# Kernel optimization log

Hardware: AMD Instinct MI355X
Metric: run time of the kernel (lower is better)

Reference implementation:

```python
import jax, jax.numpy as jnp
import numpy as np


def setup_inputs() -> dict:
    key = jax.random.key(0)
    ks = jax.random.split(key, 7)
    d, nq, nk = 64, 1024, 2048
    return {
        "query": jax.random.normal(ks[0], (1, d, nq), dtype=jnp.float32),
        "key": jax.random.normal(ks[1], (1, d, nk), dtype=jnp.float32),
        "value": jax.random.normal(ks[2], (1, d, nk), dtype=jnp.float32),
        # Conv1d(2d->d, k=1) weight squeezed to [d, 2d]; Conv1d(d->1, k=1) -> [1, d]
        "W1": jax.random.normal(ks[3], (d, 2 * d), dtype=jnp.float32) * (1.0 / np.sqrt(2 * d)),
        "b1": jax.random.normal(ks[4], (d,), dtype=jnp.float32) * 0.01,
        "W2": jax.random.normal(ks[5], (1, d), dtype=jnp.float32) * (1.0 / np.sqrt(d)),
        "b2": jax.random.normal(ks[6], (1,), dtype=jnp.float32) * 0.01,
    }


def reference(query, key, value, W1, b1, W2, b2):
    d = query.shape[1]
    # Split first conv weight into the query-half and key-half of the concat.
    # Conv1d with kernel 1 on cat([q_bcast, k_bcast]) == W1q @ q + W1k @ k (per pair).
    W1q, W1k = W1[:, :d], W1[:, d:]            # [h, d] each (h == d)
    qp = jnp.einsum('hd,bdq->bqh', W1q, query)  # [1, nq, h]
    kp = jnp.einsum('hd,bdk->bkh', W1k, key)    # [1, nk, h]
    # Pairwise hidden activations [1, nq, nk, h]
    h = jax.nn.relu(qp[:, :, None, :] + kp[:, None, :, :] + b1)
    scores = jnp.einsum('oh,bqkh->bqk', W2, h) + b2[0]  # [1, nq, nk]
    prob = jax.nn.softmax(scores, axis=-1)
    out = jnp.einsum('bnm,bdm->bdn', prob, value)        # [1, d, nq]
    return (out, scores)
```

## Files before the change

### kernel.cpp

```cpp
#include <hip/hip_runtime.h>


__global__ __launch_bounds__(256) void k1_proj(
    const float* __restrict__ q, const float* __restrict__ k,
    const float* __restrict__ W1, const float* __restrict__ b1,
    float* __restrict__ qp, float* __restrict__ kp)
{
  __shared__ float tile[256];
  const int t = threadIdx.x;
  const int b = blockIdx.x;
  if (b < 256) {
    const int nb = (b & 15) << 6;
    const int hb = (b >> 4) << 2;
    const int n = nb + (t & 63);
    const int h = hb + (t >> 6);
    const float* wr = W1 + h * 128;
    float acc = b1[h];
#pragma unroll
    for (int d = 0; d < 64; ++d) acc = fmaf(wr[d], q[(d << 10) + n], acc);
    tile[((t & 63) << 2) + (t >> 6)] = acc;
    __syncthreads();
    qp[((nb + (t >> 2)) << 6) + hb + (t & 3)] = tile[t];
  } else {
    const int b2 = b - 256;
    const int mb = (b2 & 31) << 6;
    const int hb = (b2 >> 5) << 2;
    const int m = mb + (t & 63);
    const int h = hb + (t >> 6);
    const float* wr = W1 + h * 128 + 64;
    float acc = 0.f;
#pragma unroll
    for (int d = 0; d < 64; ++d) acc = fmaf(wr[d], k[(d << 11) + m], acc);
    tile[((t & 63) << 2) + (t >> 6)] = acc;
    __syncthreads();
    kp[((mb + (t >> 2)) << 6) + hb + (t & 3)] = tile[t];
  }
}

__global__ __launch_bounds__(256, 2) void k2_scores(
    const float* __restrict__ qp, const float* __restrict__ kp,
    const float* __restrict__ W2, const float* __restrict__ b2p,
    float* __restrict__ scores, float* __restrict__ lpart)
{
  __shared__ float4 qS[1024];
  __shared__ float4 kS[1024];
  __shared__ float4 wS[16];
  const int t = threadIdx.x;
  const int qt = blockIdx.x >> 5;
  const int kt = blockIdx.x & 31;
  const int q0b = qt << 6, k0b = kt << 6;
  const float4* qp4 = (const float4*)qp;
  const float4* kp4 = (const float4*)kp;

#pragma unroll
  for (int i = 0; i < 4; ++i) {
    const int idx = (i << 8) + t;
    const int row = idx >> 4, c = idx & 15;
    const int cs = c ^ ((row >> 2) & 15);
    qS[(row << 4) + cs] = qp4[((q0b + row) << 4) + c];
    kS[(row << 4) + cs] = kp4[((k0b + row) << 4) + c];
  }
  if (t < 16) wS[t] = ((const float4*)W2)[t];
  __syncthreads();

  const int lane = t & 63, wave = t >> 6;
  const int lq = lane >> 4, lk = lane & 15;
  const int ql0 = (wave << 4) + (lq << 2);
  const int kl0 = lk << 2;
  const int sq = (wave << 2) | lq;

  float4 acc0 = {0,0,0,0}, acc1 = {0,0,0,0};
  float4 acc2 = {0,0,0,0}, acc3 = {0,0,0,0};

#pragma unroll 4
  for (int h4 = 0; h4 < 16; ++h4) {
    const float4 wv = wS[h4];
    const int qc = h4 ^ sq, kc = h4 ^ lk;
    const float4 q0f = qS[((ql0 + 0) << 4) + qc];
    const float4 q1f = qS[((ql0 + 1) << 4) + qc];
    const float4 q2f = qS[((ql0 + 2) << 4) + qc];
    const float4 q3f = qS[((ql0 + 3) << 4) + qc];
    const float4 k0f = kS[((kl0 + 0) << 4) + kc];
    const float4 k1f = kS[((kl0 + 1) << 4) + kc];
    const float4 k2f = kS[((kl0 + 2) << 4) + kc];
    const float4 k3f = kS[((kl0 + 3) << 4) + kc];
#define HC(C)                                                        \
    acc0.x = fmaf(wv.C, fmaxf(q0f.C + k0f.C, 0.f), acc0.x);          \
    acc0.y = fmaf(wv.C, fmaxf(q0f.C + k1f.C, 0.f), acc0.y);          \
    acc0.z = fmaf(wv.C, fmaxf(q0f.C + k2f.C, 0.f), acc0.z);          \
    acc0.w = fmaf(wv.C, fmaxf(q0f.C + k3f.C, 0.f), acc0.w);          \
    acc1.x = fmaf(wv.C, fmaxf(q1f.C + k0f.C, 0.f), acc1.x);          \
    acc1.y = fmaf(wv.C, fmaxf(q1f.C + k1f.C, 0.f), acc1.y);          \
    acc1.z = fmaf(wv.C, fmaxf(q1f.C + k2f.C, 0.f), acc1.z);          \
    acc1.w = fmaf(wv.C, fmaxf(q1f.C + k3f.C, 0.f), acc1.w);          \
    acc2.x = fmaf(wv.C, fmaxf(q2f.C + k0f.C, 0.f), acc2.x);          \
    acc2.y = fmaf(wv.C, fmaxf(q2f.C + k1f.C, 0.f), acc2.y);          \
    acc2.z = fmaf(wv.C, fmaxf(q2f.C + k2f.C, 0.f), acc2.z);          \
    acc2.w = fmaf(wv.C, fmaxf(q2f.C + k3f.C, 0.f), acc2.w);          \
    acc3.x = fmaf(wv.C, fmaxf(q3f.C + k0f.C, 0.f), acc3.x);          \
    acc3.y = fmaf(wv.C, fmaxf(q3f.C + k1f.C, 0.f), acc3.y);          \
    acc3.z = fmaf(wv.C, fmaxf(q3f.C + k2f.C, 0.f), acc3.z);          \
    acc3.w = fmaf(wv.C, fmaxf(q3f.C + k3f.C, 0.f), acc3.w);
    HC(x) HC(y) HC(z) HC(w)
#undef HC
  }

  const float b2v = b2p[0];
  float4* sc4 = (float4*)scores;
  const int kcol = (k0b >> 2) + lk;
#define ROW_OUT(I, ACC) {                                            \
    float4 s = ACC;                                                  \
    s.x += b2v; s.y += b2v; s.z += b2v; s.w += b2v;                  \
    sc4[((q0b + ql0 + I) << 9) + kcol] = s;                          \
    float e = __expf(s.x) + __expf(s.y) + __expf(s.z) + __expf(s.w); \
    e += __shfl_xor(e, 1); e += __shfl_xor(e, 2);                    \
    e += __shfl_xor(e, 4); e += __shfl_xor(e, 8);                    \
    if (lk == 0) lpart[(kt << 10) + q0b + ql0 + I] = e; }
  ROW_OUT(0, acc0) ROW_OUT(1, acc1) ROW_OUT(2, acc2) ROW_OUT(3, acc3)
#undef ROW_OUT
}

__global__ __launch_bounds__(256, 2) void k3_pv(
    const float* __restrict__ scores, const float* __restrict__ v,
    float* __restrict__ part)
{
  __shared__ float4 pS4[1024];
  __shared__ float4 vtS4[1024];
  float* vtSf = (float*)vtS4;
  const int t = threadIdx.x;
  const int nt = blockIdx.x >> 5;
  const int ms = blockIdx.x & 31;
  const int n0b = nt << 6;
  const int mc4 = ms << 4;

  const float4* s4 = (const float4*)scores;
  const float4* v4 = (const float4*)v;
#pragma unroll
  for (int i = 0; i < 4; ++i) {
    const int idx = (i << 8) + t;
    const int n = idx >> 4, c = idx & 15;
    float4 val = s4[((n0b + n) << 9) + mc4 + c];
    val.x = __expf(val.x); val.y = __expf(val.y);
    val.z = __expf(val.z); val.w = __expf(val.w);
    pS4[(n << 4) + c] = val;
  }
#pragma unroll
  for (int i = 0; i < 4; ++i) {
    const int idx = (i << 8) + t;
    const int dd = idx >> 4, c = idx & 15;
    const float4 val = v4[(dd << 9) + mc4 + c];
    const int co = (((dd >> 2) ^ c) << 2) + (dd & 3);
    vtSf[(c << 8) + co] = val.x;
    vtSf[(c << 8) + 64 + co] = val.y;
    vtSf[(c << 8) + 128 + co] = val.z;
    vtSf[(c << 8) + 192 + co] = val.w;
  }
  __syncthreads();

  const int tn = t >> 3, td = t & 7;
  const int n0l = tn << 1, n1l = n0l + 1;
  float4 acc00 = {0,0,0,0}, acc01 = {0,0,0,0};
  float4 acc10 = {0,0,0,0}, acc11 = {0,0,0,0};

#define PV_STEP(J, AC) {                                       \
    const float4 b0 = vtS4[(m4 << 6) + (J << 4) + c0];         \
    const float4 b1 = vtS4[(m4 << 6) + (J << 4) + (c0 ^ 8)];   \
    acc00.x = fmaf(a0.AC, b0.x, acc00.x);                      \
    acc00.y = fmaf(a0.AC, b0.y, acc00.y);                      \
    acc00.z = fmaf(a0.AC, b0.z, acc00.z);                      \
    acc00.w = fmaf(a0.AC, b0.w, acc00.w);                      \
    acc01.x = fmaf(a0.AC, b1.x, acc01.x);                      \
    acc01.y = fmaf(a0.AC, b1.y, acc01.y);                      \
    acc01.z = fmaf(a0.AC, b1.z, acc01.z);                      \
    acc01.w = fmaf(a0.AC, b1.w, acc01.w);                      \
    acc10.x = fmaf(a1.AC, b0.x, acc10.x);                      \
    acc10.y = fmaf(a1.AC, b0.y, acc10.y);                      \
    acc10.z = fmaf(a1.AC, b0.z, acc10.z);                      \
    acc10.w = fmaf(a1.AC, b0.w, acc10.w);                      \
    acc11.x = fmaf(a1.AC, b1.x, acc11.x);                      \
    acc11.y = fmaf(a1.AC, b1.y, acc11.y);                      \
    acc11.z = fmaf(a1.AC, b1.z, acc11.z);                      \
    acc11.w = fmaf(a1.AC, b1.w, acc11.w);                      \
  }

#pragma unroll
  for (int m4 = 0; m4 < 16; ++m4) {
    const float4 a0 = pS4[(n0l << 4) + m4];
    const float4 a1 = pS4[(n1l << 4) + m4];
    const int c0 = td ^ m4;
    PV_STEP(0, x) PV_STEP(1, y) PV_STEP(2, z) PV_STEP(3, w)
  }
#undef PV_STEP

  float4* part4 = (float4*)part;
  const int pb0 = (ms << 14) + ((n0b + n0l) << 4);
  const int pb1 = (ms << 14) + ((n0b + n1l) << 4);
  part4[pb0 + td] = acc00;
  part4[pb0 + td + 8] = acc01;
  part4[pb1 + td] = acc10;
  part4[pb1 + td + 8] = acc11;
}

__global__ __launch_bounds__(256) void k4_reduce(
    const float* __restrict__ part, const float* __restrict__ lpart,
    float* __restrict__ out)
{
  __shared__ float oS[256];
  const int t = threadIdx.x;
  const int nb = blockIdx.x << 2;
  const int nl = t >> 6, d = t & 63;
  const int n = nb + nl;
  float sum = 0.f;
#pragma unroll
  for (int ms = 0; ms < 32; ++ms)
    sum += part[(ms << 16) + (n << 6) + d];
  float l = 0.f;
#pragma unroll
  for (int kt = 0; kt < 32; ++kt)
    l += lpart[(kt << 10) + n];
  oS[(nl << 6) + d] = sum / l;
  __syncthreads();
  const int d2 = t >> 2, n2 = t & 3;
  out[(d2 << 10) + nb + n2] = oS[(n2 << 6) + d2];
}

extern "C" void kernel_launch(void* const* d_in, const int* in_sizes, int n_in,
                              void* d_out, int out_size, void* d_ws, size_t ws_size,
                              hipStream_t stream) {
  const float* query = (const float*)d_in[0];
  const float* key   = (const float*)d_in[1];
  const float* value = (const float*)d_in[2];
  const float* W1    = (const float*)d_in[3];
  const float* b1    = (const float*)d_in[4];
  const float* W2    = (const float*)d_in[5];
  const float* b2    = (const float*)d_in[6];

  float* out    = (float*)d_out;
  float* scores = out + 65536;

  float* ws    = (float*)d_ws;
  float* qp    = ws;
  float* kp    = ws + 65536;
  float* lpart = ws + 196608;
  float* part  = ws + 229376;

  k1_proj<<<768, 256, 0, stream>>>(query, key, W1, b1, qp, kp);
  k2_scores<<<512, 256, 0, stream>>>(qp, kp, W2, b2, scores, lpart);
  k3_pv<<<512, 256, 0, stream>>>(scores, value, part);
  k4_reduce<<<256, 256, 0, stream>>>(part, lpart, out);
}
```

Baseline: 99.92 us.

## Fuse four kernels into one cooperative persistent kernel with grid syncs

```diff
diff --git a/kernel.cpp b/kernel.cpp
--- a/kernel.cpp
+++ b/kernel.cpp
@@ -1,57 +1,61 @@
 #include <hip/hip_runtime.h>
-
-
-__global__ __launch_bounds__(256) void k1_proj(
-    const float* __restrict__ q, const float* __restrict__ k,
+#include <hip/hip_cooperative_groups.h>
+
+namespace cg = cooperative_groups;
+
+
+__global__ __launch_bounds__(256, 2) void fused_mlp_attn(
+    const float* __restrict__ q, const float* __restrict__ key,
+    const float* __restrict__ v,
     const float* __restrict__ W1, const float* __restrict__ b1,
-    float* __restrict__ qp, float* __restrict__ kp)
+    const float* __restrict__ W2, const float* __restrict__ b2p,
+    float* __restrict__ out, float* __restrict__ scores,
+    float* __restrict__ qp, float* __restrict__ kp,
+    float* __restrict__ lpart, float* __restrict__ part)
 {
-  __shared__ float tile[256];
+  __shared__ float4 smem4[2048];
+  float* smemf = (float*)smem4;
+  cg::grid_group grid = cg::this_grid();
   const int t = threadIdx.x;
-  const int b = blockIdx.x;
-  if (b < 256) {
-    const int nb = (b & 15) << 6;
-    const int hb = (b >> 4) << 2;
-    const int n = nb + (t & 63);
-    const int h = hb + (t >> 6);
-    const float* wr = W1 + h * 128;
-    float acc = b1[h];
-#pragma unroll
-    for (int d = 0; d < 64; ++d) acc = fmaf(wr[d], q[(d << 10) + n], acc);
-    tile[((t & 63) << 2) + (t >> 6)] = acc;
+  const int bid = blockIdx.x;
+
+  for (int u = bid; u < 768; u += 512) {
+    if (u < 256) {
+      const int nb = (u & 15) << 6;
+      const int hb = (u >> 4) << 2;
+      const int n = nb + (t & 63);
+      const int h = hb + (t >> 6);
+      const float* wr = W1 + h * 128;
+      float acc = b1[h];
+#pragma unroll
+      for (int d = 0; d < 64; ++d) acc = fmaf(wr[d], q[(d << 10) + n], acc);
+      smemf[((t & 63) << 2) + (t >> 6)] = acc;
+      __syncthreads();
+      qp[((nb + (t >> 2)) << 6) + hb + (t & 3)] = smemf[t];
+    } else {
+      const int u2 = u - 256;
+      const int mb = (u2 & 31) << 6;
+      const int hb = (u2 >> 5) << 2;
+      const int m = mb + (t & 63);
+      const int h = hb + (t >> 6);
+      const float* wr = W1 + h * 128 + 64;
+      float acc = 0.f;
+#pragma unroll
+      for (int d = 0; d < 64; ++d) acc = fmaf(wr[d], key[(d << 11) + m], acc);
+      smemf[((t & 63) << 2) + (t >> 6)] = acc;
+      __syncthreads();
+      kp[((mb + (t >> 2)) << 6) + hb + (t & 3)] = smemf[t];
+    }
     __syncthreads();
-    qp[((nb + (t >> 2)) << 6) + hb + (t & 3)] = tile[t];
-  } else {
-    const int b2 = b - 256;
-    const int mb = (b2 & 31) << 6;
-    const int hb = (b2 >> 5) << 2;
-    const int m = mb + (t & 63);
-    const int h = hb + (t >> 6);
-    const float* wr = W1 + h * 128 + 64;
-    float acc = 0.f;
-#pragma unroll
-    for (int d = 0; d < 64; ++d) acc = fmaf(wr[d], k[(d << 11) + m], acc);
-    tile[((t & 63) << 2) + (t >> 6)] = acc;
-    __syncthreads();
-    kp[((mb + (t >> 2)) << 6) + hb + (t & 3)] = tile[t];
-  }
-}
-
-__global__ __launch_bounds__(256, 2) void k2_scores(
-    const float* __restrict__ qp, const float* __restrict__ kp,
-    const float* __restrict__ W2, const float* __restrict__ b2p,
-    float* __restrict__ scores, float* __restrict__ lpart)
-{
-  __shared__ float4 qS[1024];
-  __shared__ float4 kS[1024];
-  __shared__ float4 wS[16];
-  const int t = threadIdx.x;
-  const int qt = blockIdx.x >> 5;
-  const int kt = blockIdx.x & 31;
+  }
+  grid.sync();
+
+  float4* qS = smem4;
+  float4* kS = smem4 + 1024;
+  const int qt = bid >> 5, kt = bid & 31;
   const int q0b = qt << 6, k0b = kt << 6;
   const float4* qp4 = (const float4*)qp;
   const float4* kp4 = (const float4*)kp;
-
 #pragma unroll
   for (int i = 0; i < 4; ++i) {
     const int idx = (i << 8) + t;
@@ -60,21 +64,21 @@
     qS[(row << 4) + cs] = qp4[((q0b + row) << 4) + c];
     kS[(row << 4) + cs] = kp4[((k0b + row) << 4) + c];
   }
-  if (t < 16) wS[t] = ((const float4*)W2)[t];
   __syncthreads();
 
   const int lane = t & 63, wave = t >> 6;
   const int lq = lane >> 4, lk = lane & 15;
   const int ql0 = (wave << 4) + (lq << 2);
+  const int sq = (wave << 2) | lq;
   const int kl0 = lk << 2;
-  const int sq = (wave << 2) | lq;
+  const float4* w24 = (const float4*)W2;
 
   float4 acc0 = {0,0,0,0}, acc1 = {0,0,0,0};
   float4 acc2 = {0,0,0,0}, acc3 = {0,0,0,0};
 
 #pragma unroll 4
   for (int h4 = 0; h4 < 16; ++h4) {
-    const float4 wv = wS[h4];
+    const float4 wv = w24[h4];
     const int qc = h4 ^ sq, kc = h4 ^ lk;
     const float4 q0f = qS[((ql0 + 0) << 4) + qc];
     const float4 q1f = qS[((ql0 + 1) << 4) + qc];
@@ -108,42 +112,31 @@
   const float b2v = b2p[0];
   float4* sc4 = (float4*)scores;
   const int kcol = (k0b >> 2) + lk;
-#define ROW_OUT(I, ACC) {                                            \
+  float4 e0, e1, e2, e3;
+#define ROW_OUT(I, ACC, E) {                                         \
     float4 s = ACC;                                                  \
     s.x += b2v; s.y += b2v; s.z += b2v; s.w += b2v;                  \
     sc4[((q0b + ql0 + I) << 9) + kcol] = s;                          \
-    float e = __expf(s.x) + __expf(s.y) + __expf(s.z) + __expf(s.w); \
+    E.x = __expf(s.x); E.y = __expf(s.y);                            \
+    E.z = __expf(s.z); E.w = __expf(s.w);                            \
+    float e = E.x + E.y + E.z + E.w;                                 \
     e += __shfl_xor(e, 1); e += __shfl_xor(e, 2);                    \
     e += __shfl_xor(e, 4); e += __shfl_xor(e, 8);                    \
     if (lk == 0) lpart[(kt << 10) + q0b + ql0 + I] = e; }
-  ROW_OUT(0, acc0) ROW_OUT(1, acc1) ROW_OUT(2, acc2) ROW_OUT(3, acc3)
+  ROW_OUT(0, acc0, e0) ROW_OUT(1, acc1, e1)
+  ROW_OUT(2, acc2, e2) ROW_OUT(3, acc3, e3)
 #undef ROW_OUT
-}
-
-__global__ __launch_bounds__(256, 2) void k3_pv(
-    const float* __restrict__ scores, const float* __restrict__ v,
-    float* __restrict__ part)
-{
-  __shared__ float4 pS4[1024];
-  __shared__ float4 vtS4[1024];
+
+  __syncthreads();
+  float4* pS4 = smem4;
+  float4* vtS4 = smem4 + 1024;
   float* vtSf = (float*)vtS4;
-  const int t = threadIdx.x;
-  const int nt = blockIdx.x >> 5;
-  const int ms = blockIdx.x & 31;
-  const int n0b = nt << 6;
-  const int mc4 = ms << 4;
-
-  const float4* s4 = (const float4*)scores;
+  pS4[((ql0 + 0) << 4) + lk] = e0;
+  pS4[((ql0 + 1) << 4) + lk] = e1;
+  pS4[((ql0 + 2) << 4) + lk] = e2;
+  pS4[((ql0 + 3) << 4) + lk] = e3;
   const float4* v4 = (const float4*)v;
-#pragma unroll
-  for (int i = 0; i < 4; ++i) {
-    const int idx = (i << 8) + t;
-    const int n = idx >> 4, c = idx & 15;
-    float4 val = s4[((n0b + n) << 9) + mc4 + c];
-    val.x = __expf(val.x); val.y = __expf(val.y);
-    val.z = __expf(val.z); val.w = __expf(val.w);
-    pS4[(n << 4) + c] = val;
-  }
+  const int mc4 = kt << 4;
 #pragma unroll
   for (int i = 0; i < 4; ++i) {
     const int idx = (i << 8) + t;
@@ -157,10 +150,11 @@
   }
   __syncthreads();
 
-  const int tn = t >> 3, td = t & 7;
-  const int n0l = tn << 1, n1l = n0l + 1;
-  float4 acc00 = {0,0,0,0}, acc01 = {0,0,0,0};
-  float4 acc10 = {0,0,0,0}, acc11 = {0,0,0,0};
+  {
+    const int tn = t >> 3, td = t & 7;
+    const int n0l = tn << 1, n1l = n0l + 1;
+    float4 acc00 = {0,0,0,0}, acc01 = {0,0,0,0};
+    float4 acc10 = {0,0,0,0}, acc11 = {0,0,0,0};
 
 #define PV_STEP(J, AC) {                                       \
     const float4 b0 = vtS4[(m4 << 6) + (J << 4) + c0];         \
@@ -184,6 +178,233 @@
   }
 
 #pragma unroll
+    for (int m4 = 0; m4 < 16; ++m4) {
+      const float4 a0 = pS4[(n0l << 4) + m4];
+      const float4 a1 = pS4[(n1l << 4) + m4];
+      const int c0 = td ^ m4;
+      PV_STEP(0, x) PV_STEP(1, y) PV_STEP(2, z) PV_STEP(3, w)
+    }
+#undef PV_STEP
+
+    float4* part4 = (float4*)part;
+    const int pb0 = (kt << 14) + ((q0b + n0l) << 4);
+    const int pb1 = (kt << 14) + ((q0b + n1l) << 4);
+    part4[pb0 + td] = acc00;
+    part4[pb0 + td + 8] = acc01;
+    part4[pb1 + td] = acc10;
+    part4[pb1 + td + 8] = acc11;
+  }
+  grid.sync();
+
+  {
+    const int nl = t >> 7;
+    const int tt = t & 127;
+    const int g = tt >> 6;
+    const int d = tt & 63;
+    const int n = (bid << 1) + nl;
+    float s = 0.f;
+#pragma unroll
+    for (int ms = 0; ms < 16; ++ms)
+      s += part[((g * 16 + ms) << 16) + (n << 6) + d];
+    smemf[(nl << 7) + (g << 6) + d] = s;
+    if (d == 0) {
+      float lp = 0.f;
+#pragma unroll
+      for (int k2 = 0; k2 < 16; ++k2) lp += lpart[((g * 16 + k2) << 10) + n];
+      smemf[512 + (nl << 1) + g] = lp;
+    }
+    __syncthreads();
+    if (t < 128) {
+      const int nl2 = t >> 6, d2 = t & 63;
+      const int n2 = (bid << 1) + nl2;
+      const float sum = smemf[(nl2 << 7) + d2] + smemf[(nl2 << 7) + 64 + d2];
+      const float l = smemf[512 + (nl2 << 1)] + smemf[512 + (nl2 << 1) + 1];
+      out[(d2 << 10) + n2] = sum / l;
+    }
+  }
+}
+
+__global__ __launch_bounds__(256) void k1_proj(
+    const float* __restrict__ q, const float* __restrict__ k,
+    const float* __restrict__ W1, const float* __restrict__ b1,
+    float* __restrict__ qp, float* __restrict__ kp)
+{
+  __shared__ float tile[256];
+  const int t = threadIdx.x;
+  const int b = blockIdx.x;
+  if (b < 256) {
+    const int nb = (b & 15) << 6;
+    const int hb = (b >> 4) << 2;
+    const int n = nb + (t & 63);
+    const int h = hb + (t >> 6);
+    const float* wr = W1 + h * 128;
+    float acc = b1[h];
+#pragma unroll
+    for (int d = 0; d < 64; ++d) acc = fmaf(wr[d], q[(d << 10) + n], acc);
+    tile[((t & 63) << 2) + (t >> 6)] = acc;
+    __syncthreads();
+    qp[((nb + (t >> 2)) << 6) + hb + (t & 3)] = tile[t];
+  } else {
+    const int b2 = b - 256;
+    const int mb = (b2 & 31) << 6;
+    const int hb = (b2 >> 5) << 2;
+    const int m = mb + (t & 63);
+    const int h = hb + (t >> 6);
+    const float* wr = W1 + h * 128 + 64;
+    float acc = 0.f;
+#pragma unroll
+    for (int d = 0; d < 64; ++d) acc = fmaf(wr[d], k[(d << 11) + m], acc);
+    tile[((t & 63) << 2) + (t >> 6)] = acc;
+    __syncthreads();
+    kp[((mb + (t >> 2)) << 6) + hb + (t & 3)] = tile[t];
+  }
+}
+
+__global__ __launch_bounds__(256, 2) void k2_scores(
+    const float* __restrict__ qp, const float* __restrict__ kp,
+    const float* __restrict__ W2, const float* __restrict__ b2p,
+    float* __restrict__ scores, float* __restrict__ lpart)
+{
+  __shared__ float4 qS[1024];
+  __shared__ float4 kS[1024];
+  const int t = threadIdx.x;
+  const int qt = blockIdx.x >> 5;
+  const int kt = blockIdx.x & 31;
+  const int q0b = qt << 6, k0b = kt << 6;
+  const float4* qp4 = (const float4*)qp;
+  const float4* kp4 = (const float4*)kp;
+#pragma unroll
+  for (int i = 0; i < 4; ++i) {
+    const int idx = (i << 8) + t;
+    const int row = idx >> 4, c = idx & 15;
+    const int cs = c ^ ((row >> 2) & 15);
+    qS[(row << 4) + cs] = qp4[((q0b + row) << 4) + c];
+    kS[(row << 4) + cs] = kp4[((k0b + row) << 4) + c];
+  }
+  __syncthreads();
+
+  const int lane = t & 63, wave = t >> 6;
+  const int lq = lane >> 4, lk = lane & 15;
+  const int ql0 = (wave << 4) + (lq << 2);
+  const int sq = (wave << 2) | lq;
+  const int kl0 = lk << 2;
+  const float4* w24 = (const float4*)W2;
+
+  float4 acc0 = {0,0,0,0}, acc1 = {0,0,0,0};
+  float4 acc2 = {0,0,0,0}, acc3 = {0,0,0,0};
+
+#pragma unroll 4
+  for (int h4 = 0; h4 < 16; ++h4) {
+    const float4 wv = w24[h4];
+    const int qc = h4 ^ sq, kc = h4 ^ lk;
+    const float4 q0f = qS[((ql0 + 0) << 4) + qc];
+    const float4 q1f = qS[((ql0 + 1) << 4) + qc];
+    const float4 q2f = qS[((ql0 + 2) << 4) + qc];
+    const float4 q3f = qS[((ql0 + 3) << 4) + qc];
+    const float4 k0f = kS[((kl0 + 0) << 4) + kc];
+    const float4 k1f = kS[((kl0 + 1) << 4) + kc];
+    const float4 k2f = kS[((kl0 + 2) << 4) + kc];
+    const float4 k3f = kS[((kl0 + 3) << 4) + kc];
+#define HC(C)                                                        \
+    acc0.x = fmaf(wv.C, fmaxf(q0f.C + k0f.C, 0.f), acc0.x);          \
+    acc0.y = fmaf(wv.C, fmaxf(q0f.C + k1f.C, 0.f), acc0.y);          \
+    acc0.z = fmaf(wv.C, fmaxf(q0f.C + k2f.C, 0.f), acc0.z);          \
+    acc0.w = fmaf(wv.C, fmaxf(q0f.C + k3f.C, 0.f), acc0.w);          \
+    acc1.x = fmaf(wv.C, fmaxf(q1f.C + k0f.C, 0.f), acc1.x);          \
+    acc1.y = fmaf(wv.C, fmaxf(q1f.C + k1f.C, 0.f), acc1.y);          \
+    acc1.z = fmaf(wv.C, fmaxf(q1f.C + k2f.C, 0.f), acc1.z);          \
+    acc1.w = fmaf(wv.C, fmaxf(q1f.C + k3f.C, 0.f), acc1.w);          \
+    acc2.x = fmaf(wv.C, fmaxf(q2f.C + k0f.C, 0.f), acc2.x);          \
+    acc2.y = fmaf(wv.C, fmaxf(q2f.C + k1f.C, 0.f), acc2.y);          \
+    acc2.z = fmaf(wv.C, fmaxf(q2f.C + k2f.C, 0.f), acc2.z);          \
+    acc2.w = fmaf(wv.C, fmaxf(q2f.C + k3f.C, 0.f), acc2.w);          \
+    acc3.x = fmaf(wv.C, fmaxf(q3f.C + k0f.C, 0.f), acc3.x);          \
+    acc3.y = fmaf(wv.C, fmaxf(q3f.C + k1f.C, 0.f), acc3.y);          \
+    acc3.z = fmaf(wv.C, fmaxf(q3f.C + k2f.C, 0.f), acc3.z);          \
+    acc3.w = fmaf(wv.C, fmaxf(q3f.C + k3f.C, 0.f), acc3.w);
+    HC(x) HC(y) HC(z) HC(w)
+#undef HC
+  }
+
+  const float b2v = b2p[0];
+  float4* sc4 = (float4*)scores;
+  const int kcol = (k0b >> 2) + lk;
+#define ROW_OUT(I, ACC) {                                            \
+    float4 s = ACC;                                                  \
+    s.x += b2v; s.y += b2v; s.z += b2v; s.w += b2v;                  \
+    sc4[((q0b + ql0 + I) << 9) + kcol] = s;                          \
+    float e = __expf(s.x) + __expf(s.y) + __expf(s.z) + __expf(s.w); \
+    e += __shfl_xor(e, 1); e += __shfl_xor(e, 2);                    \
+    e += __shfl_xor(e, 4); e += __shfl_xor(e, 8);                    \
+    if (lk == 0) lpart[(kt << 10) + q0b + ql0 + I] = e; }
+  ROW_OUT(0, acc0) ROW_OUT(1, acc1) ROW_OUT(2, acc2) ROW_OUT(3, acc3)
+#undef ROW_OUT
+}
+
+__global__ __launch_bounds__(256, 2) void k3_pv(
+    const float* __restrict__ scores, const float* __restrict__ v,
+    float* __restrict__ part)
+{
+  __shared__ float4 pS4[1024];
+  __shared__ float4 vtS4[1024];
+  float* vtSf = (float*)vtS4;
+  const int t = threadIdx.x;
+  const int nt = blockIdx.x >> 5;
+  const int ms = blockIdx.x & 31;
+  const int n0b = nt << 6;
+  const int mc4 = ms << 4;
+
+  const float4* s4 = (const float4*)scores;
+  const float4* v4 = (const float4*)v;
+#pragma unroll
+  for (int i = 0; i < 4; ++i) {
+    const int idx = (i << 8) + t;
+    const int n = idx >> 4, c = idx & 15;
+    float4 val = s4[((n0b + n) << 9) + mc4 + c];
+    val.x = __expf(val.x); val.y = __expf(val.y);
+    val.z = __expf(val.z); val.w = __expf(val.w);
+    pS4[(n << 4) + c] = val;
+  }
+#pragma unroll
+  for (int i = 0; i < 4; ++i) {
+    const int idx = (i << 8) + t;
+    const int dd = idx >> 4, c = idx & 15;
+    const float4 val = v4[(dd << 9) + mc4 + c];
+    const int co = (((dd >> 2) ^ c) << 2) + (dd & 3);
+    vtSf[(c << 8) + co] = val.x;
+    vtSf[(c << 8) + 64 + co] = val.y;
+    vtSf[(c << 8) + 128 + co] = val.z;
+    vtSf[(c << 8) + 192 + co] = val.w;
+  }
+  __syncthreads();
+
+  const int tn = t >> 3, td = t & 7;
+  const int n0l = tn << 1, n1l = n0l + 1;
+  float4 acc00 = {0,0,0,0}, acc01 = {0,0,0,0};
+  float4 acc10 = {0,0,0,0}, acc11 = {0,0,0,0};
+
+#define PV_STEP(J, AC) {                                       \
+    const float4 b0 = vtS4[(m4 << 6) + (J << 4) + c0];         \
+    const float4 b1 = vtS4[(m4 << 6) + (J << 4) + (c0 ^ 8)];   \
+    acc00.x = fmaf(a0.AC, b0.x, acc00.x);                      \
+    acc00.y = fmaf(a0.AC, b0.y, acc00.y);                      \
+    acc00.z = fmaf(a0.AC, b0.z, acc00.z);                      \
+    acc00.w = fmaf(a0.AC, b0.w, acc00.w);                      \
+    acc01.x = fmaf(a0.AC, b1.x, acc01.x);                      \
+    acc01.y = fmaf(a0.AC, b1.y, acc01.y);                      \
+    acc01.z = fmaf(a0.AC, b1.z, acc01.z);                      \
+    acc01.w = fmaf(a0.AC, b1.w, acc01.w);                      \
+    acc10.x = fmaf(a1.AC, b0.x, acc10.x);                      \
+    acc10.y = fmaf(a1.AC, b0.y, acc10.y);                      \
+    acc10.z = fmaf(a1.AC, b0.z, acc10.z);                      \
+    acc10.w = fmaf(a1.AC, b0.w, acc10.w);                      \
+    acc11.x = fmaf(a1.AC, b1.x, acc11.x);                      \
+    acc11.y = fmaf(a1.AC, b1.y, acc11.y);                      \
+    acc11.z = fmaf(a1.AC, b1.z, acc11.z);                      \
+    acc11.w = fmaf(a1.AC, b1.w, acc11.w);                      \
+  }
+
+#pragma unroll
   for (int m4 = 0; m4 < 16; ++m4) {
     const float4 a0 = pS4[(n0l << 4) + m4];
     const float4 a1 = pS4[(n1l << 4) + m4];
@@ -244,8 +465,24 @@
   float* lpart = ws + 196608;
   float* part  = ws + 229376;
 
-  k1_proj<<<768, 256, 0, stream>>>(query, key, W1, b1, qp, kp);
-  k2_scores<<<512, 256, 0, stream>>>(qp, kp, W2, b2, scores, lpart);
-  k3_pv<<<512, 256, 0, stream>>>(scores, value, part);
-  k4_reduce<<<256, 256, 0, stream>>>(part, lpart, out);
-}
+  int occ = 0, ncu = 0, dev = 0;
+  hipGetDevice(&dev);
+  hipDeviceGetAttribute(&ncu, hipDeviceAttributeMultiprocessorCount, dev);
+  hipError_t oe = hipOccupancyMaxActiveBlocksPerMultiprocessor(
+      &occ, fused_mlp_attn, 256, 0);
+
+  if (oe == hipSuccess && occ * ncu >= 512) {
+    void* args[] = {
+      (void*)&query, (void*)&key, (void*)&value, (void*)&W1, (void*)&b1,
+      (void*)&W2, (void*)&b2, (void*)&out, (void*)&scores,
+      (void*)&qp, (void*)&kp, (void*)&lpart, (void*)&part
+    };
+    hipLaunchCooperativeKernel((void*)fused_mlp_attn, dim3(512), dim3(256),
+                               args, 0, stream);
+  } else {
+    k1_proj<<<768, 256, 0, stream>>>(query, key, W1, b1, qp, kp);
+    k2_scores<<<512, 256, 0, stream>>>(qp, kp, W2, b2, scores, lpart);
+    k3_pv<<<512, 256, 0, stream>>>(scores, value, part);
+    k4_reduce<<<256, 256, 0, stream>>>(part, lpart, out);
+  }
+}
```

New measurement: 230.0 us. 2.3x slower.
